# Performance work log

Measured on AMD Instinct MI355X. Metric: run time of the kernel, lower is better.

Reference implementation:

```python
import jax, jax.numpy as jnp
import numpy as np

NH = 16  # num_attention_heads
HD = 64  # attention_head_size (hidden 1024 / 16)

def _gelu(x):
    # matches torch.jit gelu: x * 0.5 * (1 + erf(x / 1.41421))
    return x * 0.5 * (1.0 + jax.lax.erf(x / 1.41421))

def setup_inputs() -> dict:
    key = jax.random.key(0)
    ks = jax.random.split(key, 6)
    B, S, H = 32, 512, 1024
    sc = 1.0 / np.sqrt(H)
    return {
        "hidden_states": jax.random.normal(ks[0], (B, S, H), jnp.float32),
        "Wq": jax.random.normal(ks[1], (H, H), jnp.float32) * sc,
        "bq": jnp.zeros((H,), jnp.float32),
        "Wk": jax.random.normal(ks[2], (H, H), jnp.float32) * sc,
        "bk": jnp.zeros((H,), jnp.float32),
        "Wv": jax.random.normal(ks[3], (H, H), jnp.float32) * sc,
        "bv": jnp.zeros((H,), jnp.float32),
        "Wp": jax.random.normal(ks[4], (3 * S, S), jnp.float32) * (1.0 / np.sqrt(3 * S)),
        "bp": jnp.zeros((S,), jnp.float32),
    }

def reference(hidden_states, Wq, bq, Wk, bk, Wv, bv, Wp, bp):
    b, s, h = hidden_states.shape
    # transpose_for_scores in the original is a pure .view (reshape), not a permute
    q = (hidden_states @ Wq + bq).reshape(b, NH, s, HD)
    k = (hidden_states @ Wk + bk).reshape(b, NH, s, HD)
    v = (hidden_states @ Wv + bv).reshape(b, NH, s, HD)
    # pooled global value: Linear over the (3*seq) axis, then gelu
    qkv = jnp.concatenate([q, k, v], axis=-2)              # (b, nh, 3s, hd)
    gv = jnp.swapaxes(qkv, -1, -2) @ Wp + bp               # (b, nh, hd, s)
    gv = _gelu(jnp.swapaxes(gv, -1, -2))                   # (b, nh, s, hd)
    # einsum('bnij,bnji->bni', q, k^T) == per-position dot product
    local = jnp.sum(q * k, axis=-1, keepdims=True)         # (b, nh, s, 1)
    scores = jnp.concatenate([local, jnp.zeros_like(local)], axis=-1)
    scores = scores / np.sqrt(HD)                          # (b, nh, s, 2)
    probs = jax.nn.softmax(scores, axis=-1)                # dropout prob = 0 (eval)
    v2 = jnp.stack([v, gv], axis=-2)                       # (b, nh, s, 2, hd)
    ctx = jnp.einsum('bnsk,bnskd->bnsd', probs, v2)        # (b, nh, s, hd)
    ctx = jnp.transpose(ctx, (0, 2, 1, 3)).reshape(b, s, NH * HD)
    return ctx
```

## Files before the change

### kernel.cpp

```cpp
#include <hip/hip_runtime.h>


typedef unsigned short ushort_t;
typedef __attribute__((ext_vector_type(8))) short short8;
typedef __attribute__((ext_vector_type(8))) unsigned short ushort8;
typedef __attribute__((ext_vector_type(4))) float f32x4;

#define ASYNC16(gp, lp) __builtin_amdgcn_global_load_lds( \
    (const __attribute__((address_space(1))) void*)(gp),  \
    (__attribute__((address_space(3))) void*)(lp), 16, 0, 0)

__device__ __forceinline__ ushort_t f2b(float f) {
  union { float f; unsigned int u; } v; v.f = f;
  unsigned int r = v.u + 0x7FFFu + ((v.u >> 16) & 1u);
  return (ushort_t)(r >> 16);
}
__device__ __forceinline__ float b2f(ushort_t b) {
  union { unsigned int u; float f; } v; v.u = ((unsigned int)b) << 16;
  return v.f;
}

#define OFF_HSB 0ull
#define OFF_WQT (33554432ull)
#define OFF_WKT (OFF_WQT + 2097152ull)
#define OFF_WVT (OFF_WKT + 2097152ull)
#define OFF_WPT (OFF_WVT + 2097152ull)
#define OFF_QF  (OFF_WPT + 1572864ull)
#define OFF_KF  (OFF_QF + 33554432ull)
#define OFF_VF  (OFF_KF + 33554432ull)

extern "C" __global__ __launch_bounds__(256) void k_cast(
    const float* __restrict__ src, ushort_t* __restrict__ dst) {
  int i = blockIdx.x * 256 + threadIdx.x;
  const float4* s = (const float4*)src + (size_t)i * 2;
  float4 a = s[0], b = s[1];
  ushort8 o;
  o[0] = f2b(a.x); o[1] = f2b(a.y); o[2] = f2b(a.z); o[3] = f2b(a.w);
  o[4] = f2b(b.x); o[5] = f2b(b.y); o[6] = f2b(b.z); o[7] = f2b(b.w);
  *((ushort8*)dst + i) = o;
}

extern "C" __global__ __launch_bounds__(256) void k_wt(
    const float* __restrict__ s0, const float* __restrict__ s1,
    const float* __restrict__ s2, const float* __restrict__ s3,
    ushort_t* __restrict__ d0, ushort_t* __restrict__ d1,
    ushort_t* __restrict__ d2, ushort_t* __restrict__ d3) {
  int z = blockIdx.z;
  const float* src = (z == 0) ? s0 : (z == 1) ? s1 : (z == 2) ? s2 : s3;
  ushort_t* dst    = (z == 0) ? d0 : (z == 1) ? d1 : (z == 2) ? d2 : d3;
  int R = (z == 3) ? 1536 : 1024;
  int C = (z == 3) ? 512  : 1024;
  int c0 = blockIdx.x * 64, r0 = blockIdx.y * 64;
  if (c0 >= C || r0 >= R) return;
  __shared__ ushort_t tl[64][80];
  int t = threadIdx.x;
  {
    int lr = t >> 2, cg = (t & 3) * 16;
    const float* sp = src + (size_t)(r0 + lr) * C + c0 + cg;
    #pragma unroll
    for (int i = 0; i < 16; ++i) tl[lr][cg + i] = f2b(sp[i]);
  }
  __syncthreads();
  {
    int lc = t >> 2, rg = (t & 3) * 16;
    ushort_t* dp = dst + (size_t)(c0 + lc) * R + r0 + rg;
    #pragma unroll
    for (int i = 0; i < 16; ++i) dp[i] = tl[rg + i][lc];
  }
}

extern "C" __global__ __launch_bounds__(256) void k_qkv(
    const ushort_t* __restrict__ A,
    const ushort_t* __restrict__ WTq, const ushort_t* __restrict__ WTk, const ushort_t* __restrict__ WTv,
    const float* __restrict__ bq, const float* __restrict__ bk, const float* __restrict__ bv,
    ushort_t* __restrict__ Qf, ushort_t* __restrict__ Kf, ushort_t* __restrict__ Vf) {
  int z = blockIdx.z;
  const ushort_t* WT = (z == 0) ? WTq : (z == 1) ? WTk : WTv;
  const float* bias  = (z == 0) ? bq  : (z == 1) ? bk  : bv;
  ushort_t* out      = (z == 0) ? Qf  : (z == 1) ? Kf  : Vf;

  int glin = blockIdx.y * 8 + blockIdx.x;
  int nl = (glin & 7) * 128 + (glin >> 3);
  int n0 = (nl & 7) * 128, m0 = (nl >> 3) * 128;

  __shared__ ushort_t lA[128 * 32];
  __shared__ ushort_t lB[128 * 32];
  int t = threadIdx.x, lane = t & 63, wave = t >> 6;
  int wr = (wave >> 1) * 64, wc = (wave & 1) * 64;

  f32x4 acc[4][4];
  #pragma unroll
  for (int mi = 0; mi < 4; ++mi)
    #pragma unroll
    for (int ni = 0; ni < 4; ++ni)
      acc[mi][ni] = (f32x4){0.f, 0.f, 0.f, 0.f};

  for (int k0 = 0; k0 < 1024; k0 += 32) {
    #pragma unroll
    for (int j = 0; j < 2; ++j) {
      int u = j * 256 + t;
      ASYNC16(A + (size_t)(m0 + (u >> 2)) * 1024 + k0 + (u & 3) * 8,
              (char*)lA + (j * 256 + wave * 64) * 16);
    }
    #pragma unroll
    for (int j = 0; j < 2; ++j) {
      int u = j * 256 + t;
      ASYNC16(WT + (size_t)(n0 + (u >> 2)) * 1024 + k0 + (u & 3) * 8,
              (char*)lB + (j * 256 + wave * 64) * 16);
    }
    __syncthreads();
    short8 af[4], bf[4];
    #pragma unroll
    for (int mi = 0; mi < 4; ++mi)
      af[mi] = *(const short8*)&lA[(wr + mi * 16 + (lane & 15)) * 32 + (lane >> 4) * 8];
    #pragma unroll
    for (int ni = 0; ni < 4; ++ni)
      bf[ni] = *(const short8*)&lB[(wc + ni * 16 + (lane & 15)) * 32 + (lane >> 4) * 8];
    #pragma unroll
    for (int mi = 0; mi < 4; ++mi)
      #pragma unroll
      for (int ni = 0; ni < 4; ++ni)
        acc[mi][ni] = __builtin_amdgcn_mfma_f32_16x16x32_bf16(af[mi], bf[ni], acc[mi][ni], 0, 0, 0);
    __syncthreads();
  }
  #pragma unroll
  for (int ni = 0; ni < 4; ++ni) {
    int gc = n0 + wc + ni * 16 + (lane & 15);
    float bv_ = bias[gc];
    #pragma unroll
    for (int mi = 0; mi < 4; ++mi) {
      int gr = m0 + wr + mi * 16 + ((lane >> 4) << 2);
      #pragma unroll
      for (int r = 0; r < 4; ++r)
        out[(size_t)(gr + r) * 1024 + gc] = f2b(acc[mi][ni][r] + bv_);
    }
  }
}

extern "C" __global__ __launch_bounds__(256) void k_tr(
    const ushort_t* __restrict__ src, ushort_t* __restrict__ dst) {
  int bn = blockIdx.x;
  const ushort_t* s = src + (size_t)bn * 32768;
  ushort_t* d = dst + (size_t)bn * 32768;
  __shared__ ushort_t tl[64][80];
  int t = threadIdx.x;
  for (int c = 0; c < 8; ++c) {
    #pragma unroll
    for (int j = 0; j < 2; ++j) {
      int u = j * 256 + t;
      int row = u >> 3, ch = (u & 7) * 8;
      uint4 v = *(const uint4*)&s[(size_t)(c * 64 + row) * 64 + ch];
      const ushort_t* pv = (const ushort_t*)&v;
      #pragma unroll
      for (int i = 0; i < 8; ++i) tl[ch + i][row] = pv[i];
    }
    __syncthreads();
    #pragma unroll
    for (int j = 0; j < 2; ++j) {
      int u = j * 256 + t;
      int dd = u >> 3, ch = (u & 7) * 8;
      *(uint4*)&d[(size_t)dd * 512 + c * 64 + ch] = *(const uint4*)&tl[dd][ch];
    }
    __syncthreads();
  }
}

extern "C" __global__ __launch_bounds__(256) void k_p0(
    const ushort_t* __restrict__ QT, const ushort_t* __restrict__ KT,
    float* __restrict__ p0buf) {
  int bn = blockIdx.x;
  int t = threadIdx.x;
  const ushort_t* Qb = QT + (size_t)bn * 32768;
  const ushort_t* Kb = KT + (size_t)bn * 32768;
  #pragma unroll
  for (int sc = 0; sc < 2; ++sc) {
    int s = sc * 256 + t;
    float dot = 0.f;
    #pragma unroll 8
    for (int d = 0; d < 64; ++d)
      dot += b2f(Qb[d * 512 + s]) * b2f(Kb[d * 512 + s]);
    p0buf[bn * 512 + s] = 1.0f / (1.0f + __expf(-dot * 0.125f));
  }
}

extern "C" __global__ __launch_bounds__(256) void k_gv2(
    const ushort_t* __restrict__ QT, const ushort_t* __restrict__ KT, const ushort_t* __restrict__ VT,
    const ushort_t* __restrict__ WpT, const float* __restrict__ p0buf,
    const float* __restrict__ bp, float* __restrict__ out) {
  int glin = blockIdx.y * 8 + blockIdx.x;
  int nl = (glin & 7) * 128 + (glin >> 3);
  int mt = nl >> 2, nt = nl & 3;
  int m0 = mt * 128, n0 = nt * 128;

  __shared__ ushort_t lA[128 * 32];
  __shared__ ushort_t lB[128 * 32];
  int t = threadIdx.x, lane = t & 63, wave = t >> 6;
  int wr = (wave >> 1) * 64, wc = (wave & 1) * 64;

  f32x4 acc[4][4];
  #pragma unroll
  for (int mi = 0; mi < 4; ++mi)
    #pragma unroll
    for (int ni = 0; ni < 4; ++ni)
      acc[mi][ni] = (f32x4){0.f, 0.f, 0.f, 0.f};

  for (int seg = 0; seg < 3; ++seg) {
    const ushort_t* XT = (seg == 0) ? QT : (seg == 1) ? KT : VT;
    for (int kk = 0; kk < 512; kk += 32) {
      int k0 = seg * 512 + kk;
      #pragma unroll
      for (int j = 0; j < 2; ++j) {
        int u = j * 256 + t;
        int ar = m0 + (u >> 2);
        ASYNC16(XT + ((size_t)(ar >> 6) << 15) + (size_t)(ar & 63) * 512 + kk + (u & 3) * 8,
                (char*)lA + (j * 256 + wave * 64) * 16);
      }
      #pragma unroll
      for (int j = 0; j < 2; ++j) {
        int u = j * 256 + t;
        ASYNC16(WpT + (size_t)(n0 + (u >> 2)) * 1536 + k0 + (u & 3) * 8,
                (char*)lB + (j * 256 + wave * 64) * 16);
      }
      __syncthreads();
      short8 af[4], bf[4];
      #pragma unroll
      for (int mi = 0; mi < 4; ++mi)
        af[mi] = *(const short8*)&lA[(wr + mi * 16 + (lane & 15)) * 32 + (lane >> 4) * 8];
      #pragma unroll
      for (int ni = 0; ni < 4; ++ni)
        bf[ni] = *(const short8*)&lB[(wc + ni * 16 + (lane & 15)) * 32 + (lane >> 4) * 8];
      #pragma unroll
      for (int mi = 0; mi < 4; ++mi)
        #pragma unroll
        for (int ni = 0; ni < 4; ++ni)
          acc[mi][ni] = __builtin_amdgcn_mfma_f32_16x16x32_bf16(af[mi], bf[ni], acc[mi][ni], 0, 0, 0);
      __syncthreads();
    }
  }

  #pragma unroll
  for (int mi = 0; mi < 4; ++mi) {
    int r0 = m0 + wr + mi * 16 + ((lane >> 4) << 2);
    int bn = r0 >> 6, d0 = r0 & 63;
    int b = bn >> 4, nh = bn & 15;
    const ushort_t* VTb = VT + ((size_t)bn << 15);
    const float* p0row = p0buf + bn * 512;
    size_t outb = (size_t)b * 524288 + (size_t)nh * 64 + d0;
    #pragma unroll
    for (int ni = 0; ni < 4; ++ni) {
      int gc = n0 + wc + ni * 16 + (lane & 15);
      float p0 = p0row[gc];
      float bpv = bp[gc];
      float4 o;
      #pragma unroll
      for (int r = 0; r < 4; ++r) {
        float g = acc[mi][ni][r] + bpv;
        float ge = 0.5f * g * (1.0f + erff(g / 1.41421f));
        float v = b2f(VTb[(size_t)(d0 + r) * 512 + gc]);
        ((float*)&o)[r] = p0 * v + (1.0f - p0) * ge;
      }
      *(float4*)&out[outb + (size_t)gc * 1024] = o;
    }
  }
}

extern "C" void kernel_launch(void* const* d_in, const int* in_sizes, int n_in,
                              void* d_out, int out_size, void* d_ws, size_t ws_size,
                              hipStream_t stream) {
  const float* hs = (const float*)d_in[0];
  const float* Wq = (const float*)d_in[1];
  const float* bq = (const float*)d_in[2];
  const float* Wk = (const float*)d_in[3];
  const float* bk = (const float*)d_in[4];
  const float* Wv = (const float*)d_in[5];
  const float* bv = (const float*)d_in[6];
  const float* Wp = (const float*)d_in[7];
  const float* bp = (const float*)d_in[8];

  char* w = (char*)d_ws;
  ushort_t* hsb = (ushort_t*)(w + OFF_HSB);
  ushort_t* WqT = (ushort_t*)(w + OFF_WQT);
  ushort_t* WkT = (ushort_t*)(w + OFF_WKT);
  ushort_t* WvT = (ushort_t*)(w + OFF_WVT);
  ushort_t* WpT = (ushort_t*)(w + OFF_WPT);
  ushort_t* Qf  = (ushort_t*)(w + OFF_QF);
  ushort_t* Kf  = (ushort_t*)(w + OFF_KF);
  ushort_t* Vf  = (ushort_t*)(w + OFF_VF);
  ushort_t* QTt = (ushort_t*)(w + OFF_HSB);
  ushort_t* KTt = (ushort_t*)(w + OFF_QF);
  ushort_t* VTt = (ushort_t*)(w + OFF_KF);
  float*    p0b = (float*)(w + OFF_VF);

  k_cast<<<8192, 256, 0, stream>>>(hs, hsb);
  k_wt<<<dim3(16, 24, 4), 256, 0, stream>>>(Wq, Wk, Wv, Wp, WqT, WkT, WvT, WpT);
  k_qkv<<<dim3(8, 128, 3), 256, 0, stream>>>(hsb, WqT, WkT, WvT, bq, bk, bv, Qf, Kf, Vf);
  k_tr<<<512, 256, 0, stream>>>(Qf, QTt);
  k_tr<<<512, 256, 0, stream>>>(Kf, KTt);
  k_tr<<<512, 256, 0, stream>>>(Vf, VTt);
  k_p0<<<512, 256, 0, stream>>>(QTt, KTt, p0b);
  k_gv2<<<dim3(8, 128), 256, 0, stream>>>(QTt, KTt, VTt, WpT, p0b, bp, (float*)d_out);
}
```

Baseline: 402.6 us.

## Rewrite QKV GEMM as 256x256 tiled, double-buffered, swizzled 8-wave pipeline

The QKV projection GEMM now uses 256x256 output tiles with 512 threads and a 64-wide K step. Global-to-LDS async loads are double-buffered and interleaved with MFMA phases, using explicit vmcnt waits, raw barriers and setprio. LDS rows are XOR-swizzled to avoid bank conflicts. This targets the single-buffered, sync-bound 128x128 loop and raises data reuse per tile, at the cost of heavy register pressure (128 accumulator floats per thread) and large LDS use that limits occupancy.

```diff
diff --git a/kernel.cpp b/kernel.cpp
--- a/kernel.cpp
+++ b/kernel.cpp
@@ -69,7 +69,13 @@
   }
 }
 
-extern "C" __global__ __launch_bounds__(256) void k_qkv(
+#define MF(a, b, c) __builtin_amdgcn_mfma_f32_16x16x32_bf16(a, b, c, 0, 0, 0)
+#define FENCE asm volatile("" ::: "memory")
+#define BAR { FENCE; __builtin_amdgcn_s_barrier(); FENCE; }
+#define VMW(N) { asm volatile("s_waitcnt vmcnt(" #N ")" ::: "memory"); \
+                 __builtin_amdgcn_sched_barrier(0); }
+
+extern "C" __global__ __launch_bounds__(512) void k_qkv8(
     const ushort_t* __restrict__ A,
     const ushort_t* __restrict__ WTq, const ushort_t* __restrict__ WTk, const ushort_t* __restrict__ WTv,
     const float* __restrict__ bq, const float* __restrict__ bk, const float* __restrict__ bv,
@@ -79,62 +85,99 @@
   const float* bias  = (z == 0) ? bq  : (z == 1) ? bk  : bv;
   ushort_t* out      = (z == 0) ? Qf  : (z == 1) ? Kf  : Vf;
 
-  int glin = blockIdx.y * 8 + blockIdx.x;
-  int nl = (glin & 7) * 128 + (glin >> 3);
-  int n0 = (nl & 7) * 128, m0 = (nl >> 3) * 128;
-
-  __shared__ ushort_t lA[128 * 32];
-  __shared__ ushort_t lB[128 * 32];
-  int t = threadIdx.x, lane = t & 63, wave = t >> 6;
-  int wr = (wave >> 1) * 64, wc = (wave & 1) * 64;
-
-  f32x4 acc[4][4];
-  #pragma unroll
-  for (int mi = 0; mi < 4; ++mi)
-    #pragma unroll
-    for (int ni = 0; ni < 4; ++ni)
-      acc[mi][ni] = (f32x4){0.f, 0.f, 0.f, 0.f};
-
-  for (int k0 = 0; k0 < 1024; k0 += 32) {
-    #pragma unroll
-    for (int j = 0; j < 2; ++j) {
-      int u = j * 256 + t;
-      ASYNC16(A + (size_t)(m0 + (u >> 2)) * 1024 + k0 + (u & 3) * 8,
-              (char*)lA + (j * 256 + wave * 64) * 16);
-    }
-    #pragma unroll
-    for (int j = 0; j < 2; ++j) {
-      int u = j * 256 + t;
-      ASYNC16(WT + (size_t)(n0 + (u >> 2)) * 1024 + k0 + (u & 3) * 8,
-              (char*)lB + (j * 256 + wave * 64) * 16);
-    }
-    __syncthreads();
-    short8 af[4], bf[4];
-    #pragma unroll
-    for (int mi = 0; mi < 4; ++mi)
-      af[mi] = *(const short8*)&lA[(wr + mi * 16 + (lane & 15)) * 32 + (lane >> 4) * 8];
-    #pragma unroll
-    for (int ni = 0; ni < 4; ++ni)
-      bf[ni] = *(const short8*)&lB[(wc + ni * 16 + (lane & 15)) * 32 + (lane >> 4) * 8];
-    #pragma unroll
-    for (int mi = 0; mi < 4; ++mi)
-      #pragma unroll
-      for (int ni = 0; ni < 4; ++ni)
-        acc[mi][ni] = __builtin_amdgcn_mfma_f32_16x16x32_bf16(af[mi], bf[ni], acc[mi][ni], 0, 0, 0);
-    __syncthreads();
-  }
-  #pragma unroll
-  for (int ni = 0; ni < 4; ++ni) {
-    int gc = n0 + wc + ni * 16 + (lane & 15);
+  int lin = blockIdx.y * 4 + blockIdx.x;
+  int nl = (lin & 7) * 32 + (lin >> 3);
+  int m0 = (nl >> 2) * 256, n0 = (nl & 3) * 256;
+
+  __shared__ ushort_t sA[2][256 * 64];
+  __shared__ ushort_t sB[2][256 * 64];
+
+  int t = threadIdx.x, lane = t & 63, w = t >> 6;
+  int wm = w >> 2, wn = w & 3;
+  int rowA = wm * 128 + (lane & 15);
+  int rowB = wn * 64 + (lane & 15);
+  int ckh = lane >> 4;
+  int swk = lane & 7;
+
+  #define STG_A(buf, tt, h) { \
+    _Pragma("unroll") for (int j = 0; j < 2; ++j) { \
+      int u = j * 512 + t; int r = u >> 3, c = (u & 7) ^ (r & 7); \
+      ASYNC16(A + (size_t)(m0 + (h) * 128 + r) * 1024 + (tt) * 64 + c * 8, \
+              (char*)&sA[buf][0] + (h) * 16384 + (j * 512 + w * 64) * 16); } }
+  #define STG_B(buf, tt, h) { \
+    _Pragma("unroll") for (int j = 0; j < 2; ++j) { \
+      int u = j * 512 + t; int r = u >> 3, c = (u & 7) ^ (r & 7); \
+      ASYNC16(WT + (size_t)(n0 + (h) * 128 + r) * 1024 + (tt) * 64 + c * 8, \
+              (char*)&sB[buf][0] + (h) * 16384 + (j * 512 + w * 64) * 16); } }
+
+  #define LDA(buf, m, kk) (*(const short8*)((const char*)&sA[buf][0] + \
+      (((rowA + (m) * 16) * 8 + (((kk) * 4 + ckh) ^ swk)) << 4)))
+  #define LDB(buf, n, kk) (*(const short8*)((const char*)&sB[buf][0] + \
+      (((rowB + (n) * 16) * 8 + (((kk) * 4 + ckh) ^ swk)) << 4)))
+
+  #define RDA(buf, q) { a0 = LDA(buf, 2*(q), 0); a1 = LDA(buf, 2*(q), 1); \
+                        a2 = LDA(buf, 2*(q)+1, 0); a3 = LDA(buf, 2*(q)+1, 1); }
+  #define RDB(buf) { _Pragma("unroll") for (int n = 0; n < 4; ++n) { \
+                       bfr[n][0] = LDB(buf, n, 0); bfr[n][1] = LDB(buf, n, 1); } }
+  #define DOMM(q) { __builtin_amdgcn_s_setprio(1); \
+    _Pragma("unroll") for (int n = 0; n < 4; ++n) { \
+      acc[2*(q)][n]   = MF(a0, bfr[n][0], acc[2*(q)][n]); \
+      acc[2*(q)][n]   = MF(a1, bfr[n][1], acc[2*(q)][n]); \
+      acc[2*(q)+1][n] = MF(a2, bfr[n][0], acc[2*(q)+1][n]); \
+      acc[2*(q)+1][n] = MF(a3, bfr[n][1], acc[2*(q)+1][n]); } \
+    __builtin_amdgcn_s_setprio(0); }
+
+  f32x4 acc[8][4];
+  #pragma unroll
+  for (int m = 0; m < 8; ++m)
+    #pragma unroll
+    for (int n = 0; n < 4; ++n)
+      acc[m][n] = (f32x4){0.f, 0.f, 0.f, 0.f};
+  short8 bfr[4][2], a0, a1, a2, a3;
+
+  STG_B(0, 0, 0); STG_B(0, 0, 1); STG_A(0, 0, 0); STG_A(0, 0, 1);
+  STG_B(1, 1, 0); STG_B(1, 1, 1);
+  VMW(4); BAR;
+
+  for (int it = 0; it < 7; ++it) {
+    int to = 2 * it + 1, t2 = 2 * it + 2, t3 = 2 * it + 3;
+    RDB(0); RDA(0, 0); STG_A(1, to, 0); BAR; DOMM(0); BAR;
+    RDA(0, 1);         STG_A(1, to, 1); BAR; DOMM(1); BAR;
+    RDA(0, 2);         STG_B(0, t2, 0); BAR; DOMM(2); BAR;
+    RDA(0, 3);         STG_B(0, t2, 1); BAR; DOMM(3); VMW(4); BAR;
+    RDB(1); RDA(1, 0); STG_A(0, t2, 0); BAR; DOMM(0); BAR;
+    RDA(1, 1);         STG_A(0, t2, 1); BAR; DOMM(1); BAR;
+    RDA(1, 2);         STG_B(1, t3, 0); BAR; DOMM(2); BAR;
+    RDA(1, 3);         STG_B(1, t3, 1); BAR; DOMM(3); VMW(4); BAR;
+  }
+  RDB(0); RDA(0, 0); STG_A(1, 15, 0); BAR; DOMM(0); BAR;
+  RDA(0, 1);         STG_A(1, 15, 1); BAR; DOMM(1); BAR;
+  RDA(0, 2);                          BAR; DOMM(2); BAR;
+  RDA(0, 3);                          BAR; DOMM(3); VMW(0); BAR;
+  RDB(1); RDA(1, 0);                  BAR; DOMM(0); BAR;
+  RDA(1, 1);                          BAR; DOMM(1); BAR;
+  RDA(1, 2);                          BAR; DOMM(2); BAR;
+  RDA(1, 3);                          BAR; DOMM(3); BAR;
+
+  #pragma unroll
+  for (int n = 0; n < 4; ++n) {
+    int gc = n0 + wn * 64 + n * 16 + (lane & 15);
     float bv_ = bias[gc];
     #pragma unroll
-    for (int mi = 0; mi < 4; ++mi) {
-      int gr = m0 + wr + mi * 16 + ((lane >> 4) << 2);
+    for (int m = 0; m < 8; ++m) {
+      int gr = m0 + wm * 128 + m * 16 + ((lane >> 4) << 2);
       #pragma unroll
       for (int r = 0; r < 4; ++r)
-        out[(size_t)(gr + r) * 1024 + gc] = f2b(acc[mi][ni][r] + bv_);
-    }
-  }
+        out[(size_t)(gr + r) * 1024 + gc] = f2b(acc[m][n][r] + bv_);
+    }
+  }
+  #undef STG_A
+  #undef STG_B
+  #undef LDA
+  #undef LDB
+  #undef RDA
+  #undef RDB
+  #undef DOMM
 }
 
 extern "C" __global__ __launch_bounds__(256) void k_tr(
@@ -233,7 +276,7 @@
       for (int mi = 0; mi < 4; ++mi)
         #pragma unroll
         for (int ni = 0; ni < 4; ++ni)
-          acc[mi][ni] = __builtin_amdgcn_mfma_f32_16x16x32_bf16(af[mi], bf[ni], acc[mi][ni], 0, 0, 0);
+          acc[mi][ni] = MF(af[mi], bf[ni], acc[mi][ni]);
       __syncthreads();
     }
   }
@@ -293,7 +336,7 @@
 
   k_cast<<<8192, 256, 0, stream>>>(hs, hsb);
   k_wt<<<dim3(16, 24, 4), 256, 0, stream>>>(Wq, Wk, Wv, Wp, WqT, WkT, WvT, WpT);
-  k_qkv<<<dim3(8, 128, 3), 256, 0, stream>>>(hsb, WqT, WkT, WvT, bq, bk, bv, Qf, Kf, Vf);
+  k_qkv8<<<dim3(4, 64, 3), 512, 0, stream>>>(hsb, WqT, WkT, WvT, bq, bk, bv, Qf, Kf, Vf);
   k_tr<<<512, 256, 0, stream>>>(Qf, QTt);
   k_tr<<<512, 256, 0, stream>>>(Kf, KTt);
   k_tr<<<512, 256, 0, stream>>>(Vf, VTt);
```

Result: no change. 409.3 us (+1.7%).
